# Performance work log

Measured on AMD Instinct MI355X. Metric: run time of the kernel, lower is better.

Reference implementation:

```python
import jax, jax.numpy as jnp
import numpy as np

NUM_HEADS = 16
DIM = 1024


def setup_inputs() -> dict:
    key = jax.random.key(0)
    kx, kw, kb = jax.random.split(key, 3)
    x = jax.random.normal(kx, (4, 2048, DIM), dtype=jnp.float32)
    # torch Linear(dim, 3*dim): weight [3d, d], bias [3d]; store as [d, 3d] for x @ W
    W_qkv = jax.random.normal(kw, (DIM, 3 * DIM), dtype=jnp.float32) * (1.0 / np.sqrt(DIM))
    b_qkv = jax.random.normal(kb, (3 * DIM,), dtype=jnp.float32) * 0.01
    return {"x": x, "W_qkv": W_qkv, "b_qkv": b_qkv}


def reference(x, W_qkv, b_qkv):
    b, t, d = x.shape
    h = NUM_HEADS
    hd = d // h
    qkv = x @ W_qkv + b_qkv  # [b, t, 3d]
    q, k, v = jnp.split(qkv, 3, axis=-1)
    # [b, t, h, hd] -> [b, h, t, hd]
    q = q.reshape(b, t, h, hd).transpose(0, 2, 1, 3)
    k = k.reshape(b, t, h, hd).transpose(0, 2, 1, 3)
    v = v.reshape(b, t, h, hd).transpose(0, 2, 1, 3)
    # NOTE: original scales by sqrt(full dim d), not head_dim
    logits = jnp.einsum("bhqc,bhkc->bhqk", q, k) / jnp.sqrt(jnp.float32(d))
    causal = jnp.tril(jnp.ones((t, t), dtype=bool))  # [t, t]
    logits = jnp.where(causal, logits, -jnp.inf)
    attn = jax.nn.softmax(logits, axis=-1)
    out = jnp.einsum("bhqk,bhkc->bhqc", attn, v)  # [b, h, t, hd]
    return out.transpose(0, 2, 1, 3).reshape(b, t, d)
```

## Files before the change

### kernel.cpp

```cpp
#include <hip/hip_runtime.h>
#include <hip/hip_bf16.h>

#define D_MODEL 1024
#define N3      3072
#define TSEQ    2048
#define M_TOT   8192

typedef __bf16 bf16_8 __attribute__((ext_vector_type(8)));
typedef float  f32x4  __attribute__((ext_vector_type(4)));
typedef short  s16x4  __attribute__((ext_vector_type(4)));

static __device__ __forceinline__ unsigned short f2bf(float f) {
  __hip_bfloat16 h = __float2bfloat16(f);
  unsigned short u;
  __builtin_memcpy(&u, &h, 2);
  return u;
}
static __device__ __forceinline__ unsigned pack2(float lo, float hi) {
  return (unsigned)f2bf(lo) | ((unsigned)f2bf(hi) << 16);
}
static __device__ __forceinline__ void gload16(const void* g, void* l) {
  __builtin_amdgcn_global_load_lds((const __attribute__((address_space(1))) void*)g,
                                   (__attribute__((address_space(3))) void*)l, 16, 0, 0);
}

__global__ void cvt_x_kernel(const float* __restrict__ x, __bf16* __restrict__ xb) {
  size_t i = (size_t)blockIdx.x * 256 + threadIdx.x;
  float4 v = *(const float4*)(x + i * 4);
  ushort4 o;
  o.x = f2bf(v.x); o.y = f2bf(v.y); o.z = f2bf(v.z); o.w = f2bf(v.w);
  *(ushort4*)((unsigned short*)xb + i * 4) = o;
}

__global__ void cvt_w_kernel(const float* __restrict__ W, __bf16* __restrict__ WT) {
  __shared__ unsigned short tl[64][68];
  int t = threadIdx.x;
  int n0 = blockIdx.x * 64, k0 = blockIdx.y * 64;
  int rr = t >> 4, cc = (t & 15) * 4;
#pragma unroll
  for (int i = 0; i < 4; ++i) {
    int r = rr + i * 16;
    float4 v = *(const float4*)(W + (size_t)(k0 + r) * N3 + n0 + cc);
    tl[r][cc] = f2bf(v.x); tl[r][cc + 1] = f2bf(v.y);
    tl[r][cc + 2] = f2bf(v.z); tl[r][cc + 3] = f2bf(v.w);
  }
  __syncthreads();
#pragma unroll
  for (int i = 0; i < 4; ++i) {
    int rc = rr + i * 16;
    ushort4 o;
    o.x = tl[cc + 0][rc]; o.y = tl[cc + 1][rc];
    o.z = tl[cc + 2][rc]; o.w = tl[cc + 3][rc];
    *(ushort4*)((unsigned short*)WT + (size_t)(n0 + rc) * D_MODEL + k0 + cc) = o;
  }
}

__global__ void vtrans_kernel(const __bf16* __restrict__ qkv, __bf16* __restrict__ VT) {
  __shared__ unsigned short tl[64][68];
  int t = threadIdx.x;
  int t0 = blockIdx.x * 64;
  int bh = blockIdx.y;
  int b = bh >> 4, h = bh & 15;
  int rr = t >> 4, cc = (t & 15) * 4;
  const unsigned short* q16 = (const unsigned short*)qkv;
#pragma unroll
  for (int i = 0; i < 4; ++i) {
    int r = rr + i * 16;
    ushort4 v = *(const ushort4*)(q16 + (size_t)(b * TSEQ + t0 + r) * N3 + 2048 + h * 64 + cc);
    tl[r][cc] = v.x; tl[r][cc + 1] = v.y; tl[r][cc + 2] = v.z; tl[r][cc + 3] = v.w;
  }
  __syncthreads();
#pragma unroll
  for (int i = 0; i < 4; ++i) {
    int rc = rr + i * 16;
    ushort4 o;
    o.x = tl[cc + 0][rc]; o.y = tl[cc + 1][rc];
    o.z = tl[cc + 2][rc]; o.w = tl[cc + 3][rc];
    *(ushort4*)((unsigned short*)VT + (size_t)(bh * 64 + rc) * TSEQ + t0 + cc) = o;
  }
}

__global__ __launch_bounds__(256, 2) void gemm_qkv_kernel(
    const __bf16* __restrict__ A, const __bf16* __restrict__ Bt,
    const float* __restrict__ bias, __bf16* __restrict__ C) {
  __shared__ __align__(16) __bf16 Al[2][4096];
  __shared__ __align__(16) __bf16 Bl[2][4096];
  int tid = threadIdx.x;
  int wave = tid >> 6, lane = tid & 63;
  int lr = lane & 15, lg = lane >> 4;
  int m0 = blockIdx.x * 128, n0 = blockIdx.y * 128;
  int wm = (wave >> 1) * 64, wn = (wave & 1) * 64;

  const f32x4 fz = {0.f, 0.f, 0.f, 0.f};
  f32x4 acc[4][4];
#pragma unroll
  for (int i = 0; i < 4; ++i)
#pragma unroll
    for (int j = 0; j < 4; ++j) acc[i][j] = fz;

  auto stage = [&](int buf, int kt) {
#pragma unroll
    for (int call = 0; call < 2; ++call) {
      int cb = call * 256 + wave * 64;
      int c = cb + lane;
      int row = c >> 2;
      int cir = (c & 3) ^ ((row >> 1) & 3);
      gload16(A + (size_t)(m0 + row) * D_MODEL + kt * 32 + cir * 8, &Al[buf][cb * 8]);
      gload16(Bt + (size_t)(n0 + row) * D_MODEL + kt * 32 + cir * 8, &Bl[buf][cb * 8]);
    }
  };

  stage(0, 0);
  __syncthreads();
  for (int kt = 0; kt < 32; ++kt) {
    int buf = kt & 1;
    if (kt + 1 < 32) stage(buf ^ 1, kt + 1);
    bf16_8 af[4], bv[4];
#pragma unroll
    for (int mb = 0; mb < 4; ++mb) {
      int row = wm + mb * 16 + lr;
      int cir = lg ^ ((row >> 1) & 3);
      af[mb] = *(const bf16_8*)&Al[buf][row * 32 + cir * 8];
    }
#pragma unroll
    for (int nb = 0; nb < 4; ++nb) {
      int row = wn + nb * 16 + lr;
      int cir = lg ^ ((row >> 1) & 3);
      bv[nb] = *(const bf16_8*)&Bl[buf][row * 32 + cir * 8];
    }
#pragma unroll
    for (int mb = 0; mb < 4; ++mb)
#pragma unroll
      for (int nb = 0; nb < 4; ++nb)
        acc[mb][nb] = __builtin_amdgcn_mfma_f32_16x16x32_bf16(af[mb], bv[nb], acc[mb][nb], 0, 0, 0);
    __syncthreads();
  }

  const float SC = 0.04508422f;
  float oscale = (n0 < 1024) ? SC : 1.0f;
  float bvs[4];
#pragma unroll
  for (int nb = 0; nb < 4; ++nb) bvs[nb] = bias[n0 + wn + nb * 16 + lr];
  unsigned short* C16 = (unsigned short*)C;
#pragma unroll
  for (int mb = 0; mb < 4; ++mb)
#pragma unroll
    for (int nb = 0; nb < 4; ++nb)
#pragma unroll
      for (int r = 0; r < 4; ++r) {
        int row = m0 + wm + mb * 16 + lg * 4 + r;
        int col = n0 + wn + nb * 16 + lr;
        C16[(size_t)row * N3 + col] = f2bf((acc[mb][nb][r] + bvs[nb]) * oscale);
      }
}

__global__ __launch_bounds__(256, 2) void attn_kernel(
    const __bf16* __restrict__ qkv, const __bf16* __restrict__ VT,
    float* __restrict__ out) {
  __shared__ __align__(16) char smem[32768];

  int lin = blockIdx.x;
  int y = lin & 63;
  int qt = 15 - (lin >> 6);
  int bh = (y & 7) * 8 + (y >> 3);
  int b = bh >> 4, h = bh & 15;
  int tid = threadIdx.x, wave = tid >> 6, lane = tid & 63;
  int lr = lane & 15, lg = lane >> 4;
  int q0 = qt * 128 + wave * 32;

  const __bf16* Kg = qkv + (size_t)b * TSEQ * N3 + 1024 + h * 64;
  const __bf16* Vg = VT + (size_t)bh * 64 * TSEQ;

  auto stage = [&](int buf, int kv0) {
    __bf16* Kl = (__bf16*)(smem + buf * 16384);
    __bf16* Vl = (__bf16*)(smem + buf * 16384 + 8192);
#pragma unroll
    for (int call = 0; call < 2; ++call) {
      int cb = call * 256 + wave * 64;
      int c = cb + lane;
      int row = c >> 3;
      int cir = (c & 7) ^ (row & 7);
      gload16(Kg + (size_t)(kv0 + row) * N3 + cir * 8, Kl + cb * 8);
      gload16(Vg + (size_t)row * TSEQ + kv0 + cir * 8, Vl + cb * 8);
    }
  };

  bf16_8 qf[2][2];
#pragma unroll
  for (int nb = 0; nb < 2; ++nb)
#pragma unroll
    for (int kk = 0; kk < 2; ++kk)
      qf[nb][kk] = *(const bf16_8*)&qkv[(size_t)(b * TSEQ + q0 + nb * 16 + lr) * N3 + h * 64 + kk * 32 + lg * 8];

  float ps[2] = {0.f, 0.f};
  const f32x4 fz = {0.f, 0.f, 0.f, 0.f};
  f32x4 oacc[4][2];
#pragma unroll
  for (int i = 0; i < 4; ++i) { oacc[i][0] = fz; oacc[i][1] = fz; }

  int ntiles = (qt + 1) * 2;
  stage(0, 0);
  asm volatile("s_waitcnt vmcnt(0)" ::: "memory");
  __builtin_amdgcn_sched_barrier(0);
  __builtin_amdgcn_s_barrier();

  for (int tt = 0; tt < ntiles; ++tt) {
    int cur = tt & 1;
    if (tt + 1 < ntiles) stage(cur ^ 1, (tt + 1) * 64);
    __builtin_amdgcn_sched_barrier(0);

    int kv0 = tt * 64;
    if (kv0 <= q0 + 31) {
      const __bf16* Kb = (const __bf16*)(smem + cur * 16384);
      const __bf16* Vb = (const __bf16*)(smem + cur * 16384 + 8192);
      f32x4 st[4][2];
#pragma unroll
      for (int i = 0; i < 4; ++i) { st[i][0] = fz; st[i][1] = fz; }
#pragma unroll
      for (int kk = 0; kk < 2; ++kk) {
        bf16_8 kf[4];
#pragma unroll
        for (int mb = 0; mb < 4; ++mb) {
          int row = mb * 16 + lr;
          int cir = (kk * 4 + lg) ^ (row & 7);
          kf[mb] = *(const bf16_8*)&Kb[row * 64 + cir * 8];
        }
        __builtin_amdgcn_s_setprio(1);
#pragma unroll
        for (int mb = 0; mb < 4; ++mb)
#pragma unroll
          for (int nb = 0; nb < 2; ++nb)
            st[mb][nb] = __builtin_amdgcn_mfma_f32_16x16x32_bf16(kf[mb], qf[nb][kk], st[mb][nb], 0, 0, 0);
        __builtin_amdgcn_s_setprio(0);
      }
      unsigned pw[4][2][2];
      if (kv0 + 63 > q0) {
#pragma unroll
        for (int mb = 0; mb < 4; ++mb)
#pragma unroll
          for (int nb = 0; nb < 2; ++nb) {
            float p[4];
            int qq = q0 + nb * 16 + lr;
#pragma unroll
            for (int r = 0; r < 4; ++r) {
              int kv = kv0 + mb * 16 + lg * 4 + r;
              float s = (kv > qq) ? -1e30f : st[mb][nb][r];
              p[r] = __builtin_amdgcn_exp2f(s);
              ps[nb] += p[r];
            }
            pw[mb][nb][0] = pack2(p[0], p[1]);
            pw[mb][nb][1] = pack2(p[2], p[3]);
          }
      } else {
#pragma unroll
        for (int mb = 0; mb < 4; ++mb)
#pragma unroll
          for (int nb = 0; nb < 2; ++nb) {
            float p[4];
#pragma unroll
            for (int r = 0; r < 4; ++r) {
              p[r] = __builtin_amdgcn_exp2f(st[mb][nb][r]);
              ps[nb] += p[r];
            }
            pw[mb][nb][0] = pack2(p[0], p[1]);
            pw[mb][nb][1] = pack2(p[2], p[3]);
          }
      }
#pragma unroll
      for (int mb = 0; mb < 4; ++mb) {
        s16x4 vf[4];
        int chunk = mb * 2 + (lg >> 1);
#pragma unroll
        for (int mbc = 0; mbc < 4; ++mbc) {
          int row = mbc * 16 + lr;
          int cir = chunk ^ (row & 7);
          vf[mbc] = *(const s16x4*)((const char*)Vb + row * 128 + cir * 16 + (lg & 1) * 8);
        }
        __builtin_amdgcn_s_setprio(1);
#pragma unroll
        for (int nb = 0; nb < 2; ++nb) {
          union { unsigned u[2]; s16x4 v; } pf;
          pf.u[0] = pw[mb][nb][0];
          pf.u[1] = pw[mb][nb][1];
#pragma unroll
          for (int mbc = 0; mbc < 4; ++mbc)
            oacc[mbc][nb] = __builtin_amdgcn_mfma_f32_16x16x16bf16_1k(vf[mbc], pf.v, oacc[mbc][nb], 0, 0, 0);
        }
        __builtin_amdgcn_s_setprio(0);
      }
    }

    if (tt + 1 < ntiles) {
      asm volatile("s_waitcnt vmcnt(0)" ::: "memory");
      __builtin_amdgcn_sched_barrier(0);
      __builtin_amdgcn_s_barrier();
    }
  }

#pragma unroll
  for (int nb = 0; nb < 2; ++nb) {
    float s = ps[nb];
    s += __shfl_xor(s, 16, 64);
    s += __shfl_xor(s, 32, 64);
    float invl = 1.f / s;
    float* dst = out + (size_t)(b * TSEQ + q0 + nb * 16 + lr) * D_MODEL + h * 64 + lg * 4;
#pragma unroll
    for (int mbc = 0; mbc < 4; ++mbc) {
      float4 v;
      v.x = oacc[mbc][nb][0] * invl; v.y = oacc[mbc][nb][1] * invl;
      v.z = oacc[mbc][nb][2] * invl; v.w = oacc[mbc][nb][3] * invl;
      *(float4*)(dst + mbc * 16) = v;
    }
  }
}

extern "C" void kernel_launch(void* const* d_in, const int* in_sizes, int n_in,
                              void* d_out, int out_size, void* d_ws, size_t ws_size,
                              hipStream_t stream) {
  const float* x = (const float*)d_in[0];
  const float* W = (const float*)d_in[1];
  const float* bias = (const float*)d_in[2];
  float* out = (float*)d_out;
  char* ws = (char*)d_ws;
  __bf16* xb  = (__bf16*)(ws);
  __bf16* WT  = (__bf16*)(ws + (size_t)16777216);
  __bf16* qkv = (__bf16*)(ws + (size_t)23068672);
  __bf16* VT  = (__bf16*)(ws + (size_t)73400320);

  hipLaunchKernelGGL(cvt_x_kernel, dim3(8192), dim3(256), 0, stream, x, xb);
  hipLaunchKernelGGL(cvt_w_kernel, dim3(48, 16), dim3(256), 0, stream, W, WT);
  hipLaunchKernelGGL(gemm_qkv_kernel, dim3(64, 24), dim3(256), 0, stream, xb, WT, bias, qkv);
  hipLaunchKernelGGL(vtrans_kernel, dim3(32, 64), dim3(256), 0, stream, qkv, VT);
  hipLaunchKernelGGL(attn_kernel, dim3(1024), dim3(256), 0, stream, qkv, VT, out);
}
```

Before: 136.8 us.

## Enlarge QKV GEMM tiles to 256x256 with triple-buffered async LDS pipeline

The QKV projection GEMM moves from 128x128 tiles with 256 threads and double buffering to 256x256 tiles with 512 threads. It now uses a three-stage LDS ring with explicit vmcnt waits and a single barrier per k-step. A blockIdx remap groups blocks per XCD for L2 reuse, and MFMA priority is raised via setprio. The larger tiles raise arithmetic intensity and hide load latency, in exchange for 96KB of LDS, one block per CU, and higher register pressure from 32 accumulators.

After: 138.7 us. No clear change (+1.3%).

```diff
diff --git a/kernel.cpp b/kernel.cpp
--- a/kernel.cpp
+++ b/kernel.cpp
@@ -80,60 +80,72 @@
   }
 }
 
-__global__ __launch_bounds__(256, 2) void gemm_qkv_kernel(
+__global__ __launch_bounds__(512, 1) void gemm_qkv_kernel(
     const __bf16* __restrict__ A, const __bf16* __restrict__ Bt,
     const float* __restrict__ bias, __bf16* __restrict__ C) {
-  __shared__ __align__(16) __bf16 Al[2][4096];
-  __shared__ __align__(16) __bf16 Bl[2][4096];
+  __shared__ __align__(16) char smem[98304];
   int tid = threadIdx.x;
   int wave = tid >> 6, lane = tid & 63;
   int lr = lane & 15, lg = lane >> 4;
-  int m0 = blockIdx.x * 128, n0 = blockIdx.y * 128;
-  int wm = (wave >> 1) * 64, wn = (wave & 1) * 64;
+  int lin = blockIdx.x;
+  int rid = (lin & 7) * 48 + (lin >> 3);
+  int m0 = (rid & 31) * 256, n0 = (rid >> 5) * 256;
+  int wm = (wave >> 2) * 128, wn = (wave & 3) * 64;
 
   const f32x4 fz = {0.f, 0.f, 0.f, 0.f};
-  f32x4 acc[4][4];
-#pragma unroll
-  for (int i = 0; i < 4; ++i)
+  f32x4 acc[8][4];
+#pragma unroll
+  for (int i = 0; i < 8; ++i)
 #pragma unroll
     for (int j = 0; j < 4; ++j) acc[i][j] = fz;
 
   auto stage = [&](int buf, int kt) {
-#pragma unroll
-    for (int call = 0; call < 2; ++call) {
-      int cb = call * 256 + wave * 64;
+    char* Ab = smem + buf * 32768;
+    char* Bb = smem + buf * 32768 + 16384;
+#pragma unroll
+    for (int g = 0; g < 2; ++g) {
+      int cb = g * 512 + wave * 64;
       int c = cb + lane;
       int row = c >> 2;
       int cir = (c & 3) ^ ((row >> 1) & 3);
-      gload16(A + (size_t)(m0 + row) * D_MODEL + kt * 32 + cir * 8, &Al[buf][cb * 8]);
-      gload16(Bt + (size_t)(n0 + row) * D_MODEL + kt * 32 + cir * 8, &Bl[buf][cb * 8]);
+      gload16(A + (size_t)(m0 + row) * D_MODEL + kt * 32 + cir * 8, Ab + cb * 16);
+      gload16(Bt + (size_t)(n0 + row) * D_MODEL + kt * 32 + cir * 8, Bb + cb * 16);
     }
   };
 
   stage(0, 0);
-  __syncthreads();
+  stage(1, 1);
+  int cur = 0;
   for (int kt = 0; kt < 32; ++kt) {
-    int buf = kt & 1;
-    if (kt + 1 < 32) stage(buf ^ 1, kt + 1);
-    bf16_8 af[4], bv[4];
-#pragma unroll
-    for (int mb = 0; mb < 4; ++mb) {
+    if (kt < 31) asm volatile("s_waitcnt vmcnt(4)" ::: "memory");
+    else         asm volatile("s_waitcnt vmcnt(0)" ::: "memory");
+    __builtin_amdgcn_sched_barrier(0);
+    __builtin_amdgcn_s_barrier();
+    if (kt + 2 < 32) stage(cur == 0 ? 2 : cur - 1, kt + 2);
+
+    const __bf16* Ab = (const __bf16*)(smem + cur * 32768);
+    const __bf16* Bb = (const __bf16*)(smem + cur * 32768 + 16384);
+    bf16_8 af[8], bv[4];
+#pragma unroll
+    for (int mb = 0; mb < 8; ++mb) {
       int row = wm + mb * 16 + lr;
       int cir = lg ^ ((row >> 1) & 3);
-      af[mb] = *(const bf16_8*)&Al[buf][row * 32 + cir * 8];
+      af[mb] = *(const bf16_8*)&Ab[row * 32 + cir * 8];
     }
 #pragma unroll
     for (int nb = 0; nb < 4; ++nb) {
       int row = wn + nb * 16 + lr;
       int cir = lg ^ ((row >> 1) & 3);
-      bv[nb] = *(const bf16_8*)&Bl[buf][row * 32 + cir * 8];
-    }
-#pragma unroll
-    for (int mb = 0; mb < 4; ++mb)
+      bv[nb] = *(const bf16_8*)&Bb[row * 32 + cir * 8];
+    }
+    __builtin_amdgcn_s_setprio(1);
+#pragma unroll
+    for (int mb = 0; mb < 8; ++mb)
 #pragma unroll
       for (int nb = 0; nb < 4; ++nb)
         acc[mb][nb] = __builtin_amdgcn_mfma_f32_16x16x32_bf16(af[mb], bv[nb], acc[mb][nb], 0, 0, 0);
-    __syncthreads();
+    __builtin_amdgcn_s_setprio(0);
+    cur = (cur == 2) ? 0 : cur + 1;
   }
 
   const float SC = 0.04508422f;
@@ -143,7 +155,7 @@
   for (int nb = 0; nb < 4; ++nb) bvs[nb] = bias[n0 + wn + nb * 16 + lr];
   unsigned short* C16 = (unsigned short*)C;
 #pragma unroll
-  for (int mb = 0; mb < 4; ++mb)
+  for (int mb = 0; mb < 8; ++mb)
 #pragma unroll
     for (int nb = 0; nb < 4; ++nb)
 #pragma unroll
@@ -329,7 +341,7 @@
 
   hipLaunchKernelGGL(cvt_x_kernel, dim3(8192), dim3(256), 0, stream, x, xb);
   hipLaunchKernelGGL(cvt_w_kernel, dim3(48, 16), dim3(256), 0, stream, W, WT);
-  hipLaunchKernelGGL(gemm_qkv_kernel, dim3(64, 24), dim3(256), 0, stream, xb, WT, bias, qkv);
+  hipLaunchKernelGGL(gemm_qkv_kernel, dim3(384), dim3(512), 0, stream, xb, WT, bias, qkv);
   hipLaunchKernelGGL(vtrans_kernel, dim3(32, 64), dim3(256), 0, stream, qkv, VT);
   hipLaunchKernelGGL(attn_kernel, dim3(1024), dim3(256), 0, stream, qkv, VT, out);
 }
```
